# Performance work log

Hardware: AMD Instinct MI355X
Metric: run time of the kernel (lower is better)

Reference implementation:

```python
import jax, jax.numpy as jnp
import numpy as np

COST_MASK = 5.0
COST_DICE = 5.0
COST_BOX = 5.0
COST_GIOU = 2.0


def point_sample(masks, pts):
    # masks: [N, H, W]; pts: [P, 2] with (x, y) in [0, 1].
    # Matches F.grid_sample(bilinear, align_corners=False, padding_mode='zeros')
    N, H, W = masks.shape
    x = pts[:, 0] * W - 0.5
    y = pts[:, 1] * H - 0.5
    x0 = jnp.floor(x)
    y0 = jnp.floor(y)
    wx = x - x0
    wy = y - y0
    x0i = x0.astype(jnp.int32)
    y0i = y0.astype(jnp.int32)

    def gather(yi, xi):
        valid = ((xi >= 0) & (xi < W) & (yi >= 0) & (yi < H)).astype(masks.dtype)
        v = masks[:, jnp.clip(yi, 0, H - 1), jnp.clip(xi, 0, W - 1)]  # [N, P]
        return v * valid

    v00 = gather(y0i, x0i)
    v01 = gather(y0i, x0i + 1)
    v10 = gather(y0i + 1, x0i)
    v11 = gather(y0i + 1, x0i + 1)
    return (v00 * (1 - wy) * (1 - wx) + v01 * (1 - wy) * wx
            + v10 * wy * (1 - wx) + v11 * wy * wx)  # [N, P]


def box_cxcywh_to_xyxy(b):
    cx, cy, w, h = b[..., 0], b[..., 1], b[..., 2], b[..., 3]
    return jnp.stack([cx - 0.5 * w, cy - 0.5 * h, cx + 0.5 * w, cy + 0.5 * h], axis=-1)


def generalized_box_iou(a, b):
    # a: [Q, 4], b: [T, 4] in xyxy
    area_a = (a[:, 2] - a[:, 0]) * (a[:, 3] - a[:, 1])
    area_b = (b[:, 2] - b[:, 0]) * (b[:, 3] - b[:, 1])
    lt = jnp.maximum(a[:, None, :2], b[None, :, :2])
    rb = jnp.minimum(a[:, None, 2:], b[None, :, 2:])
    wh = jnp.clip(rb - lt, 0.0)
    inter = wh[..., 0] * wh[..., 1]
    union = area_a[:, None] + area_b[None, :] - inter
    iou = inter / union
    lt_e = jnp.minimum(a[:, None, :2], b[None, :, :2])
    rb_e = jnp.maximum(a[:, None, 2:], b[None, :, 2:])
    wh_e = jnp.clip(rb_e - lt_e, 0.0)
    area_e = wh_e[..., 0] * wh_e[..., 1]
    return iou - (area_e - union) / area_e


def _cost_one(out_mask, tgt_mask, out_box, tgt_box, pts):
    om = point_sample(out_mask, pts)  # [Q, P] logits
    tm = point_sample(tgt_mask, pts)  # [T, P] binary targets
    P = om.shape[1]
    # batch_sigmoid_ce_loss: BCE(x,1)=softplus(-x), BCE(x,0)=softplus(x)
    pos = jax.nn.softplus(-om)
    neg = jax.nn.softplus(om)
    cost_mask = (jnp.einsum('qp,tp->qt', pos, tm)
                 + jnp.einsum('qp,tp->qt', neg, 1.0 - tm)) / P
    # batch_dice_loss
    s = jax.nn.sigmoid(om)
    numerator = 2.0 * jnp.einsum('qp,tp->qt', s, tm)
    denominator = s.sum(-1)[:, None] + tm.sum(-1)[None, :]
    cost_dice = 1.0 - (numerator + 1.0) / (denominator + 1.0)
    # box costs
    cost_bbox = jnp.abs(out_box[:, None, :] - tgt_box[None, :, :]).sum(-1)
    cost_giou = -generalized_box_iou(box_cxcywh_to_xyxy(out_box),
                                     box_cxcywh_to_xyxy(tgt_box))
    return (COST_MASK * cost_mask + COST_DICE * cost_dice
            + COST_BOX * cost_bbox + COST_GIOU * cost_giou)


def setup_inputs() -> dict:
    key = jax.random.key(0)
    k1, k2, k3, k4, k5 = jax.random.split(key, 5)
    B, Q, T, H, W, P = 2, 300, 300, 256, 256, 12544
    pred_masks = jax.random.normal(k1, (B, Q, H, W), dtype=jnp.float32)
    tgt_masks = (jax.random.uniform(k2, (B, T, H, W)) > 0.5).astype(jnp.float32)
    u = jax.random.uniform(k3, (B, Q, 4), dtype=jnp.float32)
    pred_boxes = jnp.concatenate([0.2 + 0.6 * u[..., :2], 0.05 + 0.25 * u[..., 2:]], axis=-1)
    v = jax.random.uniform(k4, (B, T, 4), dtype=jnp.float32)
    tgt_boxes = jnp.concatenate([0.2 + 0.6 * v[..., :2], 0.05 + 0.25 * v[..., 2:]], axis=-1)
    point_coords = jax.random.uniform(k5, (B, P, 2), dtype=jnp.float32)
    return {"pred_masks": pred_masks, "tgt_masks": tgt_masks,
            "pred_boxes": pred_boxes, "tgt_boxes": tgt_boxes,
            "point_coords": point_coords}


def reference(pred_masks, tgt_masks, pred_boxes, tgt_boxes, point_coords):
    # Batched cost matrix C: [B, Q, T]
    return jax.vmap(_cost_one)(pred_masks, tgt_masks, pred_boxes, tgt_boxes, point_coords)
```

## Files before the change

### kernel.cpp

```cpp
#include <hip/hip_runtime.h>
#include <hip/hip_bf16.h>
#include <math.h>

#define BB 2
#define QQ 300
#define TT 300
#define HH 256
#define WW 256
#define PP 12544
#define NCHUNK 16
#define PBLK (PP / 256)

typedef __bf16 bf16_t;
typedef bf16_t bf16x8 __attribute__((ext_vector_type(8)));
typedef float floatx4 __attribute__((ext_vector_type(4)));

__device__ inline void gl_lds16(const void* g, void* l) {
    __builtin_amdgcn_global_load_lds(
        (const __attribute__((address_space(1))) unsigned int*)g,
        (__attribute__((address_space(3))) unsigned int*)l, 16, 0, 0);
}

__global__ __launch_bounds__(256) void prep_kernel(const float* __restrict__ pts,
                                                   int4* __restrict__ off,
                                                   float4* __restrict__ wgt,
                                                   int* __restrict__ bkt,
                                                   int* __restrict__ hist) {
    __shared__ int lh[NCHUNK];
    int tid = threadIdx.x;
    if (tid < NCHUNK) lh[tid] = 0;
    __syncthreads();
    int idx = blockIdx.x * 256 + tid;
    int b = blockIdx.x / PBLK;
    float px = pts[idx * 2 + 0];
    float py = pts[idx * 2 + 1];
    float x = px * WW - 0.5f;
    float y = py * HH - 0.5f;
    float x0f = floorf(x), y0f = floorf(y);
    float wx = x - x0f, wy = y - y0f;
    int x0 = (int)x0f, y0 = (int)y0f;
    int x1 = x0 + 1, y1 = y0 + 1;
    float vx0 = (x0 >= 0 && x0 < WW) ? 1.f : 0.f;
    float vx1 = (x1 >= 0 && x1 < WW) ? 1.f : 0.f;
    float vy0 = (y0 >= 0 && y0 < HH) ? 1.f : 0.f;
    float vy1 = (y1 >= 0 && y1 < HH) ? 1.f : 0.f;
    int cx0 = min(max(x0, 0), WW - 1), cx1 = min(max(x1, 0), WW - 1);
    int cy0 = min(max(y0, 0), HH - 1), cy1 = min(max(y1, 0), HH - 1);
    off[idx] = make_int4(cy0 * WW + cx0, cy0 * WW + cx1, cy1 * WW + cx0, cy1 * WW + cx1);
    wgt[idx] = make_float4((1.f - wy) * (1.f - wx) * vy0 * vx0,
                           (1.f - wy) * wx        * vy0 * vx1,
                           wy        * (1.f - wx) * vy1 * vx0,
                           wy        * wx         * vy1 * vx1);
    int k = min(max(y0, 0), HH - 2) >> 4;
    bkt[idx] = k;
    atomicAdd(&lh[k], 1);
    __syncthreads();
    if (tid < NCHUNK && lh[tid] > 0) atomicAdd(&hist[b * NCHUNK + tid], lh[tid]);
}

__global__ void scan_kernel(const int* __restrict__ hist, int* __restrict__ cs,
                            int* __restrict__ ctr) {
    int b = threadIdx.x;
    if (b < BB) {
        int run = 0;
        for (int k = 0; k < NCHUNK; ++k) {
            cs[b * (NCHUNK + 1) + k] = run;
            ctr[b * NCHUNK + k] = run;
            run += hist[b * NCHUNK + k];
        }
        cs[b * (NCHUNK + 1) + NCHUNK] = run;
    }
}

__global__ __launch_bounds__(256) void scatter_kernel(const int4* __restrict__ off,
                                                      const float4* __restrict__ wgt,
                                                      const int* __restrict__ bkt,
                                                      int* __restrict__ ctr,
                                                      int4* __restrict__ off_s,
                                                      float4* __restrict__ wgt_s) {
    __shared__ int lh[NCHUNK];
    __shared__ int lbase[NCHUNK];
    int tid = threadIdx.x;
    if (tid < NCHUNK) lh[tid] = 0;
    __syncthreads();
    int idx = blockIdx.x * 256 + tid;
    int b = blockIdx.x / PBLK;
    int k = bkt[idx];
    int rank = atomicAdd(&lh[k], 1);
    __syncthreads();
    if (tid < NCHUNK) lbase[tid] = (lh[tid] > 0) ? atomicAdd(&ctr[b * NCHUNK + tid], lh[tid]) : 0;
    __syncthreads();
    int pos = lbase[k] + rank;
    off_s[b * PP + pos] = off[idx];
    wgt_s[b * PP + pos] = wgt[idx];
}

__global__ __launch_bounds__(256) void sample_kernel(
    const float* __restrict__ pred_masks, const float* __restrict__ tgt_masks,
    const int4* __restrict__ off_s, const float4* __restrict__ wgt_s,
    const int* __restrict__ cs_g,
    bf16_t* __restrict__ OM, bf16_t* __restrict__ SM, bf16_t* __restrict__ TM,
    float* __restrict__ RS_SP, float* __restrict__ RS_S, float* __restrict__ RS_T) {
    int b = blockIdx.z;
    int m = blockIdx.x;
    int c = blockIdx.y;
    int tid = threadIdx.x;
    int wave = tid >> 6, lane = tid & 63;
    __shared__ __align__(16) float rows[17 * WW];
    __shared__ float ra_[4], rb_[4];

    bool is_pred = (m < QQ);
    const float* img;
    bf16_t* row0;
    bf16_t* row1 = nullptr;
    if (is_pred) {
        img  = pred_masks + (size_t)(b * QQ + m) * (HH * WW);
        row0 = OM + (size_t)(b * QQ + m) * PP;
        row1 = SM + (size_t)(b * QQ + m) * PP;
    } else {
        int t = m - QQ;
        img  = tgt_masks + (size_t)(b * TT + t) * (HH * WW);
        row0 = TM + (size_t)(b * TT + t) * PP;
    }

    int base = c * 16;
    const float4* gsrc = (const float4*)(img + base * WW);
    float4 p0 = gsrc[(wave + 0) * 64 + lane];
    float4 p1 = gsrc[(wave + 4) * 64 + lane];
    float4 p2 = gsrc[(wave + 8) * 64 + lane];
    float4 p3 = gsrc[(wave + 12) * 64 + lane];
    float4 p4;
    bool has17 = (c < NCHUNK - 1);
    if (has17 && wave == 0) p4 = gsrc[16 * 64 + lane];

    const int4*   offb = off_s + b * PP;
    const float4* wb   = wgt_s + b * PP;
    const int*    cs   = cs_g + b * (NCHUNK + 1);
    int j1 = cs[c + 1];
    int j = cs[c] + tid;
    int4 o; float4 w;
    if (j < j1) { o = offb[j]; w = wb[j]; }

    float4* d = (float4*)rows;
    d[(wave + 0) * 64 + lane] = p0;
    d[(wave + 4) * 64 + lane] = p1;
    d[(wave + 8) * 64 + lane] = p2;
    d[(wave + 12) * 64 + lane] = p3;
    if (has17 && wave == 0) d[16 * 64 + lane] = p4;
    __syncthreads();

    int boff = base * WW;
    float s0 = 0.f, s1 = 0.f;
    while (j < j1) {
        int jn = j + 256;
        int4 on; float4 wn;
        if (jn < j1) { on = offb[jn]; wn = wb[jn]; }
        float v = w.x * rows[o.x - boff] + w.y * rows[o.y - boff] +
                  w.z * rows[o.z - boff] + w.w * rows[o.w - boff];
        row0[j] = (bf16_t)v;
        if (is_pred) {
            float e = __expf(-fabsf(v));
            float r = 1.f / (1.f + e);
            float sg = (v >= 0.f) ? r : e * r;
            row1[j] = (bf16_t)sg;
            s0 += fmaxf(v, 0.f) + __logf(1.f + e);
            s1 += sg;
        } else {
            s0 += v;
        }
        o = on; w = wn; j = jn;
    }

    for (int sh = 32; sh > 0; sh >>= 1) {
        s0 += __shfl_down(s0, sh, 64);
        s1 += __shfl_down(s1, sh, 64);
    }
    if (lane == 0) { ra_[wave] = s0; rb_[wave] = s1; }
    __syncthreads();
    if (tid == 0) {
        float t0 = ra_[0] + ra_[1] + ra_[2] + ra_[3];
        float t1 = rb_[0] + rb_[1] + rb_[2] + rb_[3];
        if (is_pred) {
            atomicAdd(&RS_SP[b * QQ + m], t0);
            atomicAdd(&RS_S[b * QQ + m], t1);
        } else {
            atomicAdd(&RS_T[b * TT + (m - QQ)], t0);
        }
    }
}

template<int NS>
__global__ __launch_bounds__(512) void matmul_kernel(
    const bf16_t* __restrict__ OM, const bf16_t* __restrict__ SM, const bf16_t* __restrict__ TM,
    float* __restrict__ A1P, float* __restrict__ A2P) {
    constexpr int KSP = PP / NS;
    constexpr int KST = KSP / 64;
    static_assert(KSP % 64 == 0, "K split must be a multiple of 64");
    int b = blockIdx.z / NS;
    int split = blockIdx.z % NS;
    int m0 = blockIdx.x * 128;
    int n0 = blockIdx.y * 128;
    int tid = threadIdx.x;
    int wave = tid >> 6, lane = tid & 63;
    int lrow = lane & 15, quad = lane >> 4;
    int wm = wave & 3;
    int wn = wave >> 2;

    __shared__ __align__(16) bf16_t lds[3 * 128 * 64];

    int k0 = split * KSP;
    int lr8 = lane >> 3;
    int clog = (lane & 7) ^ lr8;

    const char* gp[6];
    unsigned lofs[6];
#pragma unroll
    for (int jj = 0; jj < 6; ++jj) {
        int L = wave + jj * 8;
        int mat = L >> 4, i = L & 15;
        int rb_ = (mat == 2) ? n0 : m0;
        int row = min(rb_ + i * 8 + lr8, (mat == 2) ? (TT - 1) : (QQ - 1));
        const bf16_t* g = (mat == 0) ? OM + (size_t)b * QQ * PP
                        : (mat == 1) ? SM + (size_t)b * QQ * PP
                                     : TM + (size_t)b * TT * PP;
        gp[jj] = (const char*)(g + (size_t)row * PP + k0) + clog * 16;
        lofs[jj] = mat * 8192 + i * 512;
    }

    floatx4 acc1[2][4], acc2[2][4];
#pragma unroll
    for (int r = 0; r < 2; ++r)
#pragma unroll
        for (int j = 0; j < 4; ++j) {
            acc1[r][j] = (floatx4){0.f, 0.f, 0.f, 0.f};
            acc2[r][j] = (floatx4){0.f, 0.f, 0.f, 0.f};
        }

    int ar0 = wm * 32 + lrow;
    int ar1 = ar0 + 16;
    int ax0 = ar0 & 7, ax1 = ar1 & 7;
    for (int s = 0; s < KST; ++s) {
#pragma unroll
        for (int jj = 0; jj < 6; ++jj) {
            gl_lds16(gp[jj], lds + lofs[jj]);
            gp[jj] += 128;
        }
        __syncthreads();
#pragma unroll
        for (int kk8 = 0; kk8 <= 4; kk8 += 4) {
            bf16x8 a1_0 = *(const bf16x8*)(lds + ar0 * 64 + (((quad + kk8) ^ ax0) << 3));
            bf16x8 a1_1 = *(const bf16x8*)(lds + ar1 * 64 + (((quad + kk8) ^ ax1) << 3));
            bf16x8 a2_0 = *(const bf16x8*)(lds + 8192 + ar0 * 64 + (((quad + kk8) ^ ax0) << 3));
            bf16x8 a2_1 = *(const bf16x8*)(lds + 8192 + ar1 * 64 + (((quad + kk8) ^ ax1) << 3));
#pragma unroll
            for (int j = 0; j < 4; ++j) {
                int br = wn * 64 + j * 16 + lrow;
                bf16x8 vb = *(const bf16x8*)(lds + 16384 + br * 64 + (((quad + kk8) ^ (br & 7)) << 3));
                acc1[0][j] = __builtin_amdgcn_mfma_f32_16x16x32_bf16(a1_0, vb, acc1[0][j], 0, 0, 0);
                acc1[1][j] = __builtin_amdgcn_mfma_f32_16x16x32_bf16(a1_1, vb, acc1[1][j], 0, 0, 0);
                acc2[0][j] = __builtin_amdgcn_mfma_f32_16x16x32_bf16(a2_0, vb, acc2[0][j], 0, 0, 0);
                acc2[1][j] = __builtin_amdgcn_mfma_f32_16x16x32_bf16(a2_1, vb, acc2[1][j], 0, 0, 0);
            }
        }
        __syncthreads();
    }

    float* o1 = A1P + (size_t)(b * NS + split) * (QQ * TT);
    float* o2 = A2P + (size_t)(b * NS + split) * (QQ * TT);
#pragma unroll
    for (int r16 = 0; r16 < 2; ++r16) {
        int mrow = m0 + wm * 32 + r16 * 16 + quad * 4;
#pragma unroll
        for (int j = 0; j < 4; ++j) {
            int n = n0 + wn * 64 + j * 16 + lrow;
            if (n < TT) {
#pragma unroll
                for (int r = 0; r < 4; ++r) {
                    int mm = mrow + r;
                    if (mm < QQ) {
                        o1[mm * TT + n] = acc1[r16][j][r];
                        o2[mm * TT + n] = acc2[r16][j][r];
                    }
                }
            }
        }
    }
}

template<int NS>
__global__ __launch_bounds__(256) void combine_kernel(
    const float* __restrict__ A1P, const float* __restrict__ A2P,
    const float* __restrict__ RS_SP, const float* __restrict__ RS_S, const float* __restrict__ RS_T,
    const float* __restrict__ pred_boxes, const float* __restrict__ tgt_boxes,
    float* __restrict__ out) {
    int idx = blockIdx.x * 256 + threadIdx.x;
    if (idx >= BB * QQ * TT) return;
    int b = idx / (QQ * TT);
    int r = idx - b * (QQ * TT);
    int q = r / TT;
    int t = r - q * TT;

    float a1 = 0.f, a2 = 0.f;
    for (int s = 0; s < NS; ++s) {
        a1 += A1P[(size_t)(b * NS + s) * (QQ * TT) + r];
        a2 += A2P[(size_t)(b * NS + s) * (QQ * TT) + r];
    }
    float cm = (RS_SP[b * QQ + q] - a1) * (1.0f / (float)PP);
    float cd = 1.f - (2.f * a2 + 1.f) / (RS_S[b * QQ + q] + RS_T[b * TT + t] + 1.f);

    const float* pb = pred_boxes + (size_t)(b * QQ + q) * 4;
    const float* tb = tgt_boxes + (size_t)(b * TT + t) * 4;
    float cb = fabsf(pb[0] - tb[0]) + fabsf(pb[1] - tb[1]) +
               fabsf(pb[2] - tb[2]) + fabsf(pb[3] - tb[3]);

    float ax0 = pb[0] - 0.5f * pb[2], ay0 = pb[1] - 0.5f * pb[3];
    float ax1 = pb[0] + 0.5f * pb[2], ay1 = pb[1] + 0.5f * pb[3];
    float bx0 = tb[0] - 0.5f * tb[2], by0 = tb[1] - 0.5f * tb[3];
    float bx1 = tb[0] + 0.5f * tb[2], by1 = tb[1] + 0.5f * tb[3];
    float area_a = (ax1 - ax0) * (ay1 - ay0);
    float area_b = (bx1 - bx0) * (by1 - by0);
    float iw = fmaxf(fminf(ax1, bx1) - fmaxf(ax0, bx0), 0.f);
    float ih = fmaxf(fminf(ay1, by1) - fmaxf(ay0, by0), 0.f);
    float inter = iw * ih;
    float uni = area_a + area_b - inter;
    float iou = inter / uni;
    float ew = fmaxf(ax1, bx1) - fminf(ax0, bx0);
    float eh = fmaxf(ay1, by1) - fminf(ay0, by0);
    float area_e = ew * eh;
    float giou = iou - (area_e - uni) / area_e;

    out[idx] = 5.f * cm + 5.f * cd + 5.f * cb - 2.f * giou;
}

extern "C" void kernel_launch(void* const* d_in, const int* in_sizes, int n_in,
                              void* d_out, int out_size, void* d_ws, size_t ws_size,
                              hipStream_t stream) {
    const float* pred_masks = (const float*)d_in[0];
    const float* tgt_masks  = (const float*)d_in[1];
    const float* pred_boxes = (const float*)d_in[2];
    const float* tgt_boxes  = (const float*)d_in[3];
    const float* pts        = (const float*)d_in[4];

    char* w = (char*)d_ws;
    auto alloc = [&](size_t bytes) -> char* {
        char* r = w;
        w += (bytes + 255) & ~(size_t)255;
        return r;
    };
    int4*   OFF   = (int4*)  alloc((size_t)BB * PP * sizeof(int4));
    float4* WGT   = (float4*)alloc((size_t)BB * PP * sizeof(float4));
    int*    BKT   = (int*)   alloc((size_t)BB * PP * sizeof(int));
    int4*   OFF_S = (int4*)  alloc((size_t)BB * PP * sizeof(int4));
    float4* WGT_S = (float4*)alloc((size_t)BB * PP * sizeof(float4));
    int*    CS    = (int*)   alloc((size_t)BB * (NCHUNK + 1) * sizeof(int));
    bf16_t* OM    = (bf16_t*)alloc((size_t)BB * QQ * PP * 2);
    bf16_t* SM    = (bf16_t*)alloc((size_t)BB * QQ * PP * 2);
    bf16_t* TM    = (bf16_t*)alloc((size_t)BB * TT * PP * 2);
    float*  RS_SP = (float*) alloc((size_t)BB * QQ * 4);
    float*  RS_S  = (float*) alloc((size_t)BB * QQ * 4);
    float*  RS_T  = (float*) alloc((size_t)BB * TT * 4);
    int*    HIST  = (int*)   alloc((size_t)BB * NCHUNK * sizeof(int));
    int*    CTR   = (int*)   alloc((size_t)BB * NCHUNK * sizeof(int));

    size_t used = (size_t)(w - (char*)d_ws);
    size_t per_arr28 = (size_t)BB * 28 * QQ * TT * 4;
    int NS = (ws_size >= used + 2 * per_arr28 + 4096) ? 28 : 14;
    float* A1P = (float*)alloc((size_t)BB * NS * QQ * TT * 4);
    float* A2P = (float*)alloc((size_t)BB * NS * QQ * TT * 4);

    hipMemsetAsync(RS_SP, 0, (size_t)((char*)A1P - (char*)RS_SP), stream);

    prep_kernel<<<BB * PBLK, 256, 0, stream>>>(pts, OFF, WGT, BKT, HIST);
    scan_kernel<<<1, 64, 0, stream>>>(HIST, CS, CTR);
    scatter_kernel<<<BB * PBLK, 256, 0, stream>>>(OFF, WGT, BKT, CTR, OFF_S, WGT_S);
    sample_kernel<<<dim3(QQ + TT, NCHUNK, BB), 256, 0, stream>>>(
        pred_masks, tgt_masks, OFF_S, WGT_S, CS, OM, SM, TM, RS_SP, RS_S, RS_T);
    if (NS == 28) {
        matmul_kernel<28><<<dim3(3, 3, BB * 28), 512, 0, stream>>>(OM, SM, TM, A1P, A2P);
        combine_kernel<28><<<(BB * QQ * TT + 255) / 256, 256, 0, stream>>>(
            A1P, A2P, RS_SP, RS_S, RS_T, pred_boxes, tgt_boxes, (float*)d_out);
    } else {
        matmul_kernel<14><<<dim3(3, 3, BB * 14), 512, 0, stream>>>(OM, SM, TM, A1P, A2P);
        combine_kernel<14><<<(BB * QQ * TT + 255) / 256, 256, 0, stream>>>(
            A1P, A2P, RS_SP, RS_S, RS_T, pred_boxes, tgt_boxes, (float*)d_out);
    }
}
```

Baseline: 374.9 us.

## Recompute sigmoid inside matmul, drop SM buffer, double-buffer LDS loads

The sample kernel no longer writes a separate bf16 sigmoid matrix. The matmul now recomputes the sigmoid from the logits held in LDS (sigmoid8) and loads only two operand tiles per step into a double-buffered LDS, with explicit vmcnt/lgkmcnt barriers so the next tile's global loads overlap with the MFMAs. The K split is fixed at 14. This removes a full write and read of a Q×P bf16 matrix, paying with extra exp/div work in the MFMA inner loop, which is recomputed for each tile column. Sigmoid of a bf16-rounded logit also differs slightly from the earlier fp32-derived value.

```diff
diff --git a/kernel.cpp b/kernel.cpp
--- a/kernel.cpp
+++ b/kernel.cpp
@@ -10,6 +10,7 @@
 #define PP 12544
 #define NCHUNK 16
 #define PBLK (PP / 256)
+#define NSPLIT 14
 
 typedef __bf16 bf16_t;
 typedef bf16_t bf16x8 __attribute__((ext_vector_type(8)));
@@ -20,6 +21,20 @@
         (const __attribute__((address_space(1))) unsigned int*)g,
         (__attribute__((address_space(3))) unsigned int*)l, 16, 0, 0);
 }
+
+#define LG_BAR() do {                                      \
+    __builtin_amdgcn_sched_barrier(0);                     \
+    asm volatile("s_waitcnt lgkmcnt(0)" ::: "memory");     \
+    __builtin_amdgcn_s_barrier();                          \
+    __builtin_amdgcn_sched_barrier(0);                     \
+} while (0)
+
+#define VM_BAR(N) do {                                     \
+    __builtin_amdgcn_sched_barrier(0);                     \
+    asm volatile("s_waitcnt vmcnt(" #N ")" ::: "memory");  \
+    __builtin_amdgcn_s_barrier();                          \
+    __builtin_amdgcn_sched_barrier(0);                     \
+} while (0)
 
 __global__ __launch_bounds__(256) void prep_kernel(const float* __restrict__ pts,
                                                    int4* __restrict__ off,
@@ -99,7 +114,7 @@
     const float* __restrict__ pred_masks, const float* __restrict__ tgt_masks,
     const int4* __restrict__ off_s, const float4* __restrict__ wgt_s,
     const int* __restrict__ cs_g,
-    bf16_t* __restrict__ OM, bf16_t* __restrict__ SM, bf16_t* __restrict__ TM,
+    bf16_t* __restrict__ OM, bf16_t* __restrict__ TM,
     float* __restrict__ RS_SP, float* __restrict__ RS_S, float* __restrict__ RS_T) {
     int b = blockIdx.z;
     int m = blockIdx.x;
@@ -112,11 +127,9 @@
     bool is_pred = (m < QQ);
     const float* img;
     bf16_t* row0;
-    bf16_t* row1 = nullptr;
     if (is_pred) {
         img  = pred_masks + (size_t)(b * QQ + m) * (HH * WW);
         row0 = OM + (size_t)(b * QQ + m) * PP;
-        row1 = SM + (size_t)(b * QQ + m) * PP;
     } else {
         int t = m - QQ;
         img  = tgt_masks + (size_t)(b * TT + t) * (HH * WW);
@@ -162,7 +175,6 @@
             float e = __expf(-fabsf(v));
             float r = 1.f / (1.f + e);
             float sg = (v >= 0.f) ? r : e * r;
-            row1[j] = (bf16_t)sg;
             s0 += fmaxf(v, 0.f) + __logf(1.f + e);
             s1 += sg;
         } else {
@@ -189,9 +201,21 @@
     }
 }
 
+__device__ inline bf16x8 sigmoid8(bf16x8 a) {
+    bf16x8 r;
+#pragma unroll
+    for (int i = 0; i < 8; ++i) {
+        float x = (float)a[i];
+        float e = __expf(-fabsf(x));
+        float q = 1.f / (1.f + e);
+        r[i] = (bf16_t)((x >= 0.f) ? q : e * q);
+    }
+    return r;
+}
+
 template<int NS>
 __global__ __launch_bounds__(512) void matmul_kernel(
-    const bf16_t* __restrict__ OM, const bf16_t* __restrict__ SM, const bf16_t* __restrict__ TM,
+    const bf16_t* __restrict__ OM, const bf16_t* __restrict__ TM,
     float* __restrict__ A1P, float* __restrict__ A2P) {
     constexpr int KSP = PP / NS;
     constexpr int KST = KSP / 64;
@@ -206,23 +230,21 @@
     int wm = wave & 3;
     int wn = wave >> 2;
 
-    __shared__ __align__(16) bf16_t lds[3 * 128 * 64];
+    __shared__ __align__(16) bf16_t lds[2][2 * 128 * 64];
 
     int k0 = split * KSP;
     int lr8 = lane >> 3;
     int clog = (lane & 7) ^ lr8;
 
-    const char* gp[6];
-    unsigned lofs[6];
-#pragma unroll
-    for (int jj = 0; jj < 6; ++jj) {
+    const char* gp[4];
+    unsigned lofs[4];
+#pragma unroll
+    for (int jj = 0; jj < 4; ++jj) {
         int L = wave + jj * 8;
         int mat = L >> 4, i = L & 15;
-        int rb_ = (mat == 2) ? n0 : m0;
-        int row = min(rb_ + i * 8 + lr8, (mat == 2) ? (TT - 1) : (QQ - 1));
-        const bf16_t* g = (mat == 0) ? OM + (size_t)b * QQ * PP
-                        : (mat == 1) ? SM + (size_t)b * QQ * PP
-                                     : TM + (size_t)b * TT * PP;
+        int rb_ = mat ? n0 : m0;
+        int row = min(rb_ + i * 8 + lr8, mat ? (TT - 1) : (QQ - 1));
+        const bf16_t* g = mat ? TM + (size_t)b * TT * PP : OM + (size_t)b * QQ * PP;
         gp[jj] = (const char*)(g + (size_t)row * PP + k0) + clog * 16;
         lofs[jj] = mat * 8192 + i * 512;
     }
@@ -235,34 +257,39 @@
             acc1[r][j] = (floatx4){0.f, 0.f, 0.f, 0.f};
             acc2[r][j] = (floatx4){0.f, 0.f, 0.f, 0.f};
         }
+
+#pragma unroll
+    for (int jj = 0; jj < 4; ++jj) { gl_lds16(gp[jj], lds[0] + lofs[jj]); gp[jj] += 128; }
 
     int ar0 = wm * 32 + lrow;
     int ar1 = ar0 + 16;
     int ax0 = ar0 & 7, ax1 = ar1 & 7;
     for (int s = 0; s < KST; ++s) {
-#pragma unroll
-        for (int jj = 0; jj < 6; ++jj) {
-            gl_lds16(gp[jj], lds + lofs[jj]);
-            gp[jj] += 128;
-        }
-        __syncthreads();
+        if (s + 1 < KST) {
+#pragma unroll
+            for (int jj = 0; jj < 4; ++jj) { gl_lds16(gp[jj], lds[(s + 1) & 1] + lofs[jj]); gp[jj] += 128; }
+            VM_BAR(4);
+        } else {
+            VM_BAR(0);
+        }
+        const bf16_t* Lp = lds[s & 1];
 #pragma unroll
         for (int kk8 = 0; kk8 <= 4; kk8 += 4) {
-            bf16x8 a1_0 = *(const bf16x8*)(lds + ar0 * 64 + (((quad + kk8) ^ ax0) << 3));
-            bf16x8 a1_1 = *(const bf16x8*)(lds + ar1 * 64 + (((quad + kk8) ^ ax1) << 3));
-            bf16x8 a2_0 = *(const bf16x8*)(lds + 8192 + ar0 * 64 + (((quad + kk8) ^ ax0) << 3));
-            bf16x8 a2_1 = *(const bf16x8*)(lds + 8192 + ar1 * 64 + (((quad + kk8) ^ ax1) << 3));
+            bf16x8 a1_0 = *(const bf16x8*)(Lp + ar0 * 64 + (((quad + kk8) ^ ax0) << 3));
+            bf16x8 a1_1 = *(const bf16x8*)(Lp + ar1 * 64 + (((quad + kk8) ^ ax1) << 3));
+            bf16x8 a2_0 = sigmoid8(a1_0);
+            bf16x8 a2_1 = sigmoid8(a1_1);
 #pragma unroll
             for (int j = 0; j < 4; ++j) {
                 int br = wn * 64 + j * 16 + lrow;
-                bf16x8 vb = *(const bf16x8*)(lds + 16384 + br * 64 + (((quad + kk8) ^ (br & 7)) << 3));
+                bf16x8 vb = *(const bf16x8*)(Lp + 8192 + br * 64 + (((quad + kk8) ^ (br & 7)) << 3));
                 acc1[0][j] = __builtin_amdgcn_mfma_f32_16x16x32_bf16(a1_0, vb, acc1[0][j], 0, 0, 0);
                 acc1[1][j] = __builtin_amdgcn_mfma_f32_16x16x32_bf16(a1_1, vb, acc1[1][j], 0, 0, 0);
                 acc2[0][j] = __builtin_amdgcn_mfma_f32_16x16x32_bf16(a2_0, vb, acc2[0][j], 0, 0, 0);
                 acc2[1][j] = __builtin_amdgcn_mfma_f32_16x16x32_bf16(a2_1, vb, acc2[1][j], 0, 0, 0);
             }
         }
-        __syncthreads();
+        LG_BAR();
     }
 
     float* o1 = A1P + (size_t)(b * NS + split) * (QQ * TT);
@@ -354,19 +381,14 @@
     float4* WGT_S = (float4*)alloc((size_t)BB * PP * sizeof(float4));
     int*    CS    = (int*)   alloc((size_t)BB * (NCHUNK + 1) * sizeof(int));
     bf16_t* OM    = (bf16_t*)alloc((size_t)BB * QQ * PP * 2);
-    bf16_t* SM    = (bf16_t*)alloc((size_t)BB * QQ * PP * 2);
     bf16_t* TM    = (bf16_t*)alloc((size_t)BB * TT * PP * 2);
     float*  RS_SP = (float*) alloc((size_t)BB * QQ * 4);
     float*  RS_S  = (float*) alloc((size_t)BB * QQ * 4);
     float*  RS_T  = (float*) alloc((size_t)BB * TT * 4);
     int*    HIST  = (int*)   alloc((size_t)BB * NCHUNK * sizeof(int));
     int*    CTR   = (int*)   alloc((size_t)BB * NCHUNK * sizeof(int));
-
-    size_t used = (size_t)(w - (char*)d_ws);
-    size_t per_arr28 = (size_t)BB * 28 * QQ * TT * 4;
-    int NS = (ws_size >= used + 2 * per_arr28 + 4096) ? 28 : 14;
-    float* A1P = (float*)alloc((size_t)BB * NS * QQ * TT * 4);
-    float* A2P = (float*)alloc((size_t)BB * NS * QQ * TT * 4);
+    float*  A1P   = (float*) alloc((size_t)BB * NSPLIT * QQ * TT * 4);
+    float*  A2P   = (float*) alloc((size_t)BB * NSPLIT * QQ * TT * 4);
 
     hipMemsetAsync(RS_SP, 0, (size_t)((char*)A1P - (char*)RS_SP), stream);
 
@@ -374,14 +396,8 @@
     scan_kernel<<<1, 64, 0, stream>>>(HIST, CS, CTR);
     scatter_kernel<<<BB * PBLK, 256, 0, stream>>>(OFF, WGT, BKT, CTR, OFF_S, WGT_S);
     sample_kernel<<<dim3(QQ + TT, NCHUNK, BB), 256, 0, stream>>>(
-        pred_masks, tgt_masks, OFF_S, WGT_S, CS, OM, SM, TM, RS_SP, RS_S, RS_T);
-    if (NS == 28) {
-        matmul_kernel<28><<<dim3(3, 3, BB * 28), 512, 0, stream>>>(OM, SM, TM, A1P, A2P);
-        combine_kernel<28><<<(BB * QQ * TT + 255) / 256, 256, 0, stream>>>(
-            A1P, A2P, RS_SP, RS_S, RS_T, pred_boxes, tgt_boxes, (float*)d_out);
-    } else {
-        matmul_kernel<14><<<dim3(3, 3, BB * 14), 512, 0, stream>>>(OM, SM, TM, A1P, A2P);
-        combine_kernel<14><<<(BB * QQ * TT + 255) / 256, 256, 0, stream>>>(
-            A1P, A2P, RS_SP, RS_S, RS_T, pred_boxes, tgt_boxes, (float*)d_out);
-    }
-}
+        pred_masks, tgt_masks, OFF_S, WGT_S, CS, OM, TM, RS_SP, RS_S, RS_T);
+    matmul_kernel<NSPLIT><<<dim3(3, 3, BB * NSPLIT), 512, 0, stream>>>(OM, TM, A1P, A2P);
+    combine_kernel<NSPLIT><<<(BB * QQ * TT + 255) / 256, 256, 0, stream>>>(
+        A1P, A2P, RS_SP, RS_S, RS_T, pred_boxes, tgt_boxes, (float*)d_out);
+}
```

Measured after the change: 393.2 us. 4.9% more time.
